# Performance work log

Hardware: AMD Instinct MI355X
Metric: run time of the kernel (lower is better)

Reference implementation:

```python
import jax, jax.numpy as jnp
import numpy as np

K = 3  # dynamic kernel size


def _conv(x, w, b, pad):
    # x: [B,Cin,H,W], w: [Cout,Cin,kh,kw]
    y = jax.lax.conv_general_dilated(
        x, w, window_strides=(1, 1), padding=pad,
        dimension_numbers=("NCHW", "OIHW", "NCHW"))
    return y + b[None, :, None, None]


def setup_inputs() -> dict:
    key = jax.random.key(0)
    ks = jax.random.split(key, 9)
    B, C, H, W = 16, 256, 64, 64
    sc1 = 1.0 / np.sqrt(C * 9)
    sc3 = 1.0 / np.sqrt(C)
    return {
        "x":    jax.random.normal(ks[0], (B, C, H, W), jnp.float32),
        "kin":  jax.random.normal(ks[1], (B, C, H, W), jnp.float32),
        "w1":   jax.random.normal(ks[2], (C, C, 3, 3), jnp.float32) * sc1,
        "b1":   jax.random.normal(ks[3], (C,), jnp.float32) * 0.01,
        "w2":   jax.random.normal(ks[4], (C, C, 3, 3), jnp.float32) * sc1,
        "b2":   jax.random.normal(ks[5], (C,), jnp.float32) * 0.01,
        "w3":   jax.random.normal(ks[6], (K * K * C, C, 1, 1), jnp.float32) * sc3,
        "b3":   jax.random.normal(ks[7], (K * K * C,), jnp.float32) * 0.01,
        "bias": jax.random.normal(ks[8], (C,), jnp.float32) * 0.01,
    }


def reference(x, kin, w1, b1, w2, b2, w3, b3, bias):
    B, C, H, W = x.shape
    # tokernel: conv3x3 (valid) -> lrelu(0.1) -> conv3x3 -> lrelu -> global avg pool -> 1x1 conv
    h = jax.nn.leaky_relu(_conv(kin, w1, b1, "VALID"), 0.1)
    h = jax.nn.leaky_relu(_conv(h, w2, b2, "VALID"), 0.1)
    p = h.mean(axis=(2, 3))                                   # [B,C] adaptive avg pool 1x1
    kern = jnp.einsum("bc,oc->bo", p, w3.reshape(K * K * C, C)) + b3  # 1x1 conv
    kern = kern.reshape(B, C, 1, K, K)                        # per-sample depthwise weights

    pad = [(K // 2, K // 2)] * 2

    def dw(xi, wi):  # xi: [C,H,W], wi: [C,1,K,K]
        return jax.lax.conv_general_dilated(
            xi[None], wi, window_strides=(1, 1), padding=pad,
            dimension_numbers=("NCHW", "OIHW", "NCHW"),
            feature_group_count=C)[0]

    y = jax.vmap(dw)(x, kern)                                 # [B,C,H,W]
    return y + bias[None, :, None, None]
```

## Files before the change

### kernel.cpp

```cpp
#include <hip/hip_runtime.h>
#include <hip/hip_bf16.h>
#include <stdint.h>

#define CCH 256

typedef __attribute__((ext_vector_type(8))) short short8;
typedef __attribute__((ext_vector_type(4))) float f32x4;

__device__ __forceinline__ float lrelu(float v) { return v > 0.f ? v : 0.1f * v; }

__device__ __forceinline__ unsigned short f2bf(float f) {
    __hip_bfloat16 h = __float2bfloat16(f);
    return *reinterpret_cast<unsigned short*>(&h);
}

__device__ __forceinline__ void gl_lds16(const void* g, void* s) {
    __builtin_amdgcn_global_load_lds(
        (const __attribute__((address_space(1))) unsigned int*)(uintptr_t)g,
        (__attribute__((address_space(3))) unsigned int*)(unsigned int)(uintptr_t)s,
        16, 0, 0);
}

__global__ __launch_bounds__(256)
void nhwc_k(const float* __restrict__ in, unsigned short* __restrict__ out)
{
    __shared__ float t[32][65];
    const int tid = threadIdx.x;
    const int kc = blockIdx.x, y = blockIdx.y, b = blockIdx.z;
    const float* src = in + ((size_t)(b * 256 + kc * 32)) * 4096 + y * 64;
#pragma unroll
    for (int i = 0; i < 2; ++i) {
        int idx = tid + i * 256;
        int cl = idx >> 4, xg = idx & 15;
        float4 v = *(const float4*)(src + (size_t)cl * 4096 + xg * 4);
        t[cl][xg * 4 + 0] = v.x; t[cl][xg * 4 + 1] = v.y;
        t[cl][xg * 4 + 2] = v.z; t[cl][xg * 4 + 3] = v.w;
    }
    __syncthreads();
    const int x = tid >> 2, cg = tid & 3;
    union { unsigned short us[8]; uint4 v; } u;
#pragma unroll
    for (int j = 0; j < 8; ++j) u.us[j] = f2bf(t[cg * 8 + j][x]);
    unsigned short* dst = out + (((size_t)(b * 8 + kc) * 4096 + y * 64 + x) * 32 + cg * 8);
    *(uint4*)dst = u.v;
}

__global__ __launch_bounds__(256)
void wtr_k(const float* __restrict__ w1, const float* __restrict__ w2,
           unsigned short* __restrict__ o1, unsigned short* __restrict__ o2)
{
    const int kc = blockIdx.x / 9, t = blockIdx.x - kc * 9;
    const float* w = blockIdx.y ? w2 : w1;
    unsigned short* o = blockIdx.y ? o2 : o1;
    const int co = threadIdx.x;
#pragma unroll
    for (int q = 0; q < 4; ++q) {
        union { unsigned short us[8]; uint4 v; } u;
#pragma unroll
        for (int uu = 0; uu < 8; ++uu)
            u.us[uu] = f2bf(w[((size_t)co * 256 + kc * 32 + q * 8 + uu) * 9 + t]);
        *(uint4*)(o + ((size_t)((kc * 9 + t) * 4 + q)) * 2048 + co * 8) = u.v;
    }
}

__global__ __launch_bounds__(256)
void zero_pool_k(float* __restrict__ p) { p[blockIdx.x * 256 + threadIdx.x] = 0.f; }

template<int POOL, int WIN, int WOUT>
__global__ __launch_bounds__(256, 2)
void convmm_k(const unsigned short* __restrict__ im, const unsigned short* __restrict__ wt,
              const float* __restrict__ bias, unsigned short* __restrict__ outp,
              float* __restrict__ pool)
{
    constexpr int HINPIX = WIN * WIN;
    constexpr int NVAL   = WOUT * WOUT;
    __shared__ __align__(16) short Ls[2 * 4 * 2056 + 2 * 4 * 1032];

    const int tid  = threadIdx.x;
    const int wave = tid >> 6;
    const int lane = tid & 63;
    const int quad = lane >> 4;
    const int l15  = lane & 15;
    const int wm   = (wave & 1) * 128;
    const int wn   = (wave >> 1) * 64;
    const int nb0  = blockIdx.x * 128;
    const int b    = blockIdx.y;

    short* const Aq = Ls;
    short* const Bq = Ls + 2 * 4 * 2056;

    const unsigned short* abase = wt + (size_t)wave * 2048 + (size_t)lane * 8;
    size_t bofs[2];
#pragma unroll
    for (int h = 0; h < 2; ++h) {
        int nn = nb0 + h * 64 + lane;
        if (nn > NVAL - 1) nn = NVAL - 1;
        int y = nn / WOUT, x = nn - y * WOUT;
        bofs[h] = ((size_t)(b * 8) * HINPIX + (size_t)y * WIN + x) * 32 + wave * 8;
    }

    f32x4 acc[8][4];
#pragma unroll
    for (int i = 0; i < 8; ++i)
#pragma unroll
        for (int j = 0; j < 4; ++j) { f32x4 z = {0.f, 0.f, 0.f, 0.f}; acc[i][j] = z; }

    for (int s = 0; s < 72; s += 2) {
#pragma unroll
        for (int u = 0; u < 2; ++u) {
            const int ss = s + u;
            const int kc = ss / 9, t = ss - kc * 9;
            const int ky = t / 3, kx = t - ky * 3;
            const size_t aoff = (size_t)ss * 8192;
            const size_t boff = ((size_t)kc * HINPIX + ky * WIN + kx) * 32;
            short* al = Aq + (u * 4 + wave) * 2056;
            short* bl = Bq + (u * 4 + wave) * 1032;
#pragma unroll
            for (int h = 0; h < 4; ++h)
                gl_lds16(abase + aoff + h * 512, al + h * 512);
#pragma unroll
            for (int h = 0; h < 2; ++h)
                gl_lds16(im + bofs[h] + boff, bl + h * 512);
        }
        __syncthreads();
#pragma unroll
        for (int u = 0; u < 2; ++u) {
            const short* ap = Aq + (u * 4 + quad) * 2056;
            const short* bp = Bq + (u * 4 + quad) * 1032;
            short8 a[8], bf[4];
#pragma unroll
            for (int i = 0; i < 8; ++i)
                a[i]  = *(const short8*)(ap + (wm + i * 16 + l15) * 8);
#pragma unroll
            for (int j = 0; j < 4; ++j)
                bf[j] = *(const short8*)(bp + (wn + j * 16 + l15) * 8);
#pragma unroll
            for (int i = 0; i < 8; ++i)
#pragma unroll
                for (int j = 0; j < 4; ++j)
                    acc[i][j] = __builtin_amdgcn_mfma_f32_16x16x32_bf16(a[i], bf[j], acc[i][j], 0, 0, 0);
        }
        __syncthreads();
    }

    const int co_l = wm + quad * 4;
    if (!POOL) {
#pragma unroll
        for (int i = 0; i < 8; ++i) {
            const int c0 = co_l + i * 16;
            float4 bv = *(const float4*)(bias + c0);
            unsigned short* dstp = outp + ((size_t)(b * 8 + (c0 >> 5)) * NVAL) * 32 + (c0 & 31);
#pragma unroll
            for (int j = 0; j < 4; ++j) {
                int nn = nb0 + wn + j * 16 + l15;
                if (nn < NVAL) {
                    ushort4 pk = make_ushort4(
                        f2bf(lrelu(acc[i][j].x + bv.x)),
                        f2bf(lrelu(acc[i][j].y + bv.y)),
                        f2bf(lrelu(acc[i][j].z + bv.z)),
                        f2bf(lrelu(acc[i][j].w + bv.w)));
                    *(ushort4*)(dstp + (size_t)nn * 32) = pk;
                }
            }
        }
    } else {
#pragma unroll
        for (int i = 0; i < 8; ++i) {
            const int c0 = co_l + i * 16;
            float4 bv = *(const float4*)(bias + c0);
            float s0 = 0.f, s1 = 0.f, s2 = 0.f, s3 = 0.f;
#pragma unroll
            for (int j = 0; j < 4; ++j) {
                int nn = nb0 + wn + j * 16 + l15;
                if (nn < NVAL) {
                    s0 += lrelu(acc[i][j].x + bv.x);
                    s1 += lrelu(acc[i][j].y + bv.y);
                    s2 += lrelu(acc[i][j].z + bv.z);
                    s3 += lrelu(acc[i][j].w + bv.w);
                }
            }
#pragma unroll
            for (int off = 1; off < 16; off <<= 1) {
                s0 += __shfl_xor(s0, off, 64);
                s1 += __shfl_xor(s1, off, 64);
                s2 += __shfl_xor(s2, off, 64);
                s3 += __shfl_xor(s3, off, 64);
            }
            if (l15 == 0) {
                float* pp = pool + b * 256 + c0;
                atomicAdd(pp + 0, s0); atomicAdd(pp + 1, s1);
                atomicAdd(pp + 2, s2); atomicAdd(pp + 3, s3);
            }
        }
    }
}

__global__ __launch_bounds__(256)
void kern_gemm_k(const float* __restrict__ p, const float* __restrict__ w3,
                 const float* __restrict__ b3, float* __restrict__ kern)
{
    const int b = blockIdx.y;
    const int o = blockIdx.x * 256 + threadIdx.x;
    __shared__ float pv[CCH];
    pv[threadIdx.x] = p[b * CCH + threadIdx.x] * (1.f / 3600.f);
    __syncthreads();
    float acc = b3[o];
    const float* wr = w3 + (size_t)o * CCH;
#pragma unroll 4
    for (int c = 0; c < CCH; c += 4) {
        float4 wv = *(const float4*)(wr + c);
        acc += wv.x * pv[c] + wv.y * pv[c + 1] + wv.z * pv[c + 2] + wv.w * pv[c + 3];
    }
    kern[(size_t)b * (9 * CCH) + o] = acc;
}

__global__ __launch_bounds__(256)
void dw_k(const float* __restrict__ x, const float* __restrict__ kern,
          const float* __restrict__ bias, float* __restrict__ out)
{
    __shared__ float t[66 * 67];
    const int tid = threadIdx.x;
    const int bc = blockIdx.x;
    const int c = bc & (CCH - 1);
    const int b = bc >> 8;

#pragma unroll
    for (int i = 0; i < 18; ++i) {
        int idx = tid + i * 256;
        if (idx < 66 * 67) t[idx] = 0.f;
    }

    const float* kp = kern + (size_t)b * (9 * CCH) + c * 9;
    float k[9];
#pragma unroll
    for (int q = 0; q < 9; ++q) k[q] = kp[q];
    const float bs = bias[c];
    const float* xp = x + (size_t)bc * 4096;
    float* op = out + (size_t)bc * 4096;
    __syncthreads();

#pragma unroll
    for (int i = 0; i < 4; ++i) {
        int p4 = tid + i * 256;
        float4 v = *(const float4*)(xp + p4 * 4);
        int yy = p4 >> 4, xx = (p4 & 15) * 4;
        float* d = &t[(yy + 1) * 67 + 1 + xx];
        d[0] = v.x; d[1] = v.y; d[2] = v.z; d[3] = v.w;
    }
    __syncthreads();

#pragma unroll
    for (int i = 0; i < 4; ++i) {
        int p4 = tid + i * 256;
        int yy = p4 >> 4, xx = (p4 & 15) * 4;
        float r[3][6];
#pragma unroll
        for (int dy = 0; dy < 3; ++dy)
#pragma unroll
            for (int dx = 0; dx < 6; ++dx)
                r[dy][dx] = t[(yy + dy) * 67 + xx + dx];
        float4 o;
        float* ov = (float*)&o;
#pragma unroll
        for (int j = 0; j < 4; ++j) {
            float a = bs;
#pragma unroll
            for (int dy = 0; dy < 3; ++dy)
#pragma unroll
                for (int dx = 0; dx < 3; ++dx)
                    a += k[dy * 3 + dx] * r[dy][j + dx];
            ov[j] = a;
        }
        *(float4*)(op + p4 * 4) = o;
    }
}

extern "C" void kernel_launch(void* const* d_in, const int* in_sizes, int n_in,
                              void* d_out, int out_size, void* d_ws, size_t ws_size,
                              hipStream_t stream)
{
    const float* x    = (const float*)d_in[0];
    const float* kin  = (const float*)d_in[1];
    const float* w1   = (const float*)d_in[2];
    const float* b1   = (const float*)d_in[3];
    const float* w2   = (const float*)d_in[4];
    const float* b2   = (const float*)d_in[5];
    const float* w3   = (const float*)d_in[6];
    const float* b3   = (const float*)d_in[7];
    const float* bias = (const float*)d_in[8];

    unsigned short* imA = (unsigned short*)d_ws;
    unsigned short* h1  = imA + (size_t)16 * 8 * 4096 * 32;
    unsigned short* w1t = h1 + (size_t)16 * 8 * 3844 * 32 + 8192;
    unsigned short* w2t = w1t + (size_t)72 * 4 * 2048;
    float* pool = (float*)(w2t + (size_t)72 * 4 * 2048);
    float* kern = pool + 16 * 256;

    float* out = (float*)d_out;

    hipLaunchKernelGGL(zero_pool_k, dim3(16), dim3(256), 0, stream, pool);
    hipLaunchKernelGGL(nhwc_k, dim3(8, 64, 16), dim3(256), 0, stream, kin, imA);
    hipLaunchKernelGGL(wtr_k, dim3(72, 2), dim3(256), 0, stream, w1, w2, w1t, w2t);
    hipLaunchKernelGGL((convmm_k<0, 64, 62>), dim3(31, 16), dim3(256), 0, stream,
                       imA, w1t, b1, h1, (float*)nullptr);
    hipLaunchKernelGGL((convmm_k<1, 62, 60>), dim3(29, 16), dim3(256), 0, stream,
                       h1, w2t, b2, (unsigned short*)nullptr, pool);
    hipLaunchKernelGGL(kern_gemm_k, dim3(9, 16), dim3(256), 0, stream, pool, w3, b3, kern);
    hipLaunchKernelGGL(dw_k, dim3(16 * 256), dim3(256), 0, stream, x, kern, bias, out);
}
```

Measured before the change: 353.1 us.

## Triple-buffer conv GEMM LDS staging with one barrier per stage

Replaces the two-stage-load, sync, compute, sync loop in the implicit-GEMM conv kernel with a three-buffer software pipeline. Global-to-LDS loads for stage s+2 are issued before computing stage s, with partial vmcnt waits and a single raw barrier per iteration. MFMA bursts are wrapped in s_setprio. The goal is to hide global load latency behind MFMA work, at the cost of about 1.5x the LDS footprint, which may reduce occupancy at 2 blocks per CU.

```diff
diff --git a/kernel.cpp b/kernel.cpp
--- a/kernel.cpp
+++ b/kernel.cpp
@@ -19,6 +19,12 @@
         (const __attribute__((address_space(1))) unsigned int*)(uintptr_t)g,
         (__attribute__((address_space(3))) unsigned int*)(unsigned int)(uintptr_t)s,
         16, 0, 0);
+}
+
+__device__ __forceinline__ void pipe_barrier() {
+    asm volatile("" ::: "memory");
+    __builtin_amdgcn_s_barrier();
+    asm volatile("" ::: "memory");
 }
 
 __global__ __launch_bounds__(256)
@@ -74,7 +80,8 @@
 {
     constexpr int HINPIX = WIN * WIN;
     constexpr int NVAL   = WOUT * WOUT;
-    __shared__ __align__(16) short Ls[2 * 4 * 2056 + 2 * 4 * 1032];
+    constexpr int NB = 4 * 2056 + 4 * 1032;
+    __shared__ __align__(16) short Ls[3 * NB];
 
     const int tid  = threadIdx.x;
     const int wave = tid >> 6;
@@ -86,9 +93,6 @@
     const int nb0  = blockIdx.x * 128;
     const int b    = blockIdx.y;
 
-    short* const Aq = Ls;
-    short* const Bq = Ls + 2 * 4 * 2056;
-
     const unsigned short* abase = wt + (size_t)wave * 2048 + (size_t)lane * 8;
     size_t bofs[2];
 #pragma unroll
@@ -105,51 +109,69 @@
 #pragma unroll
         for (int j = 0; j < 4; ++j) { f32x4 z = {0.f, 0.f, 0.f, 0.f}; acc[i][j] = z; }
 
-    for (int s = 0; s < 72; s += 2) {
-#pragma unroll
-        for (int u = 0; u < 2; ++u) {
-            const int ss = s + u;
-            const int kc = ss / 9, t = ss - kc * 9;
-            const int ky = t / 3, kx = t - ky * 3;
-            const size_t aoff = (size_t)ss * 8192;
-            const size_t boff = ((size_t)kc * HINPIX + ky * WIN + kx) * 32;
-            short* al = Aq + (u * 4 + wave) * 2056;
-            short* bl = Bq + (u * 4 + wave) * 1032;
-#pragma unroll
-            for (int h = 0; h < 4; ++h)
-                gl_lds16(abase + aoff + h * 512, al + h * 512);
-#pragma unroll
-            for (int h = 0; h < 2; ++h)
-                gl_lds16(im + bofs[h] + boff, bl + h * 512);
-        }
-        __syncthreads();
-#pragma unroll
-        for (int u = 0; u < 2; ++u) {
-            const short* ap = Aq + (u * 4 + quad) * 2056;
-            const short* bp = Bq + (u * 4 + quad) * 1032;
-            short8 a[8], bf[4];
-#pragma unroll
-            for (int i = 0; i < 8; ++i)
-                a[i]  = *(const short8*)(ap + (wm + i * 16 + l15) * 8);
+    auto stage = [&](int ss, short* buf) {
+        const int kc = ss / 9, t = ss - kc * 9;
+        const int ky = t / 3, kx = t - ky * 3;
+        const size_t aoff = (size_t)ss * 8192;
+        const size_t boff = ((size_t)kc * HINPIX + (size_t)ky * WIN + kx) * 32;
+        short* al = buf + wave * 2056;
+        short* bl = buf + 4 * 2056 + wave * 1032;
+#pragma unroll
+        for (int h = 0; h < 4; ++h)
+            gl_lds16(abase + aoff + h * 512, al + h * 512);
+#pragma unroll
+        for (int h = 0; h < 2; ++h)
+            gl_lds16(im + bofs[h] + boff, bl + h * 512);
+    };
+
+    auto compute = [&](const short* buf) {
+        const short* ap = buf + quad * 2056;
+        const short* bp = buf + 4 * 2056 + quad * 1032;
+        short8 a[8], bfr[4];
+#pragma unroll
+        for (int i = 0; i < 8; ++i)
+            a[i]  = *(const short8*)(ap + (wm + i * 16 + l15) * 8);
+#pragma unroll
+        for (int j = 0; j < 4; ++j)
+            bfr[j] = *(const short8*)(bp + (wn + j * 16 + l15) * 8);
+        __builtin_amdgcn_s_setprio(1);
+#pragma unroll
+        for (int i = 0; i < 8; ++i)
 #pragma unroll
             for (int j = 0; j < 4; ++j)
-                bf[j] = *(const short8*)(bp + (wn + j * 16 + l15) * 8);
-#pragma unroll
-            for (int i = 0; i < 8; ++i)
-#pragma unroll
-                for (int j = 0; j < 4; ++j)
-                    acc[i][j] = __builtin_amdgcn_mfma_f32_16x16x32_bf16(a[i], bf[j], acc[i][j], 0, 0, 0);
-        }
-        __syncthreads();
-    }
+                acc[i][j] = __builtin_amdgcn_mfma_f32_16x16x32_bf16(a[i], bfr[j], acc[i][j], 0, 0, 0);
+        __builtin_amdgcn_s_setprio(0);
+    };
+
+    short* B0 = Ls;
+    short* B1 = Ls + NB;
+    short* B2 = Ls + 2 * NB;
+
+    stage(0, B0);
+    stage(1, B1);
+    asm volatile("s_waitcnt vmcnt(6)" ::: "memory");
+    pipe_barrier();
+
+    short *c0 = B0, *c1 = B1, *c2 = B2;
+    for (int s = 0; s < 70; ++s) {
+        stage(s + 2, c2);
+        compute(c0);
+        asm volatile("s_waitcnt vmcnt(6)" ::: "memory");
+        pipe_barrier();
+        short* t = c0; c0 = c1; c1 = c2; c2 = t;
+    }
+    compute(c0);
+    asm volatile("s_waitcnt vmcnt(0)" ::: "memory");
+    pipe_barrier();
+    compute(c1);
 
     const int co_l = wm + quad * 4;
     if (!POOL) {
 #pragma unroll
         for (int i = 0; i < 8; ++i) {
-            const int c0 = co_l + i * 16;
-            float4 bv = *(const float4*)(bias + c0);
-            unsigned short* dstp = outp + ((size_t)(b * 8 + (c0 >> 5)) * NVAL) * 32 + (c0 & 31);
+            const int c0i = co_l + i * 16;
+            float4 bv = *(const float4*)(bias + c0i);
+            unsigned short* dstp = outp + ((size_t)(b * 8 + (c0i >> 5)) * NVAL) * 32 + (c0i & 31);
 #pragma unroll
             for (int j = 0; j < 4; ++j) {
                 int nn = nb0 + wn + j * 16 + l15;
@@ -166,8 +188,8 @@
     } else {
 #pragma unroll
         for (int i = 0; i < 8; ++i) {
-            const int c0 = co_l + i * 16;
-            float4 bv = *(const float4*)(bias + c0);
+            const int c0i = co_l + i * 16;
+            float4 bv = *(const float4*)(bias + c0i);
             float s0 = 0.f, s1 = 0.f, s2 = 0.f, s3 = 0.f;
 #pragma unroll
             for (int j = 0; j < 4; ++j) {
@@ -187,7 +209,7 @@
                 s3 += __shfl_xor(s3, off, 64);
             }
             if (l15 == 0) {
-                float* pp = pool + b * 256 + c0;
+                float* pp = pool + b * 256 + c0i;
                 atomicAdd(pp + 0, s0); atomicAdd(pp + 1, s1);
                 atomicAdd(pp + 2, s2); atomicAdd(pp + 3, s3);
             }
```

Result: faster. 341.0 us (-3.4%).
